# Kernel optimization log

Measured on AMD Instinct MI355X. Metric: run time of the kernel, lower is better.

## Reference

```python
import jax, jax.numpy as jnp
import numpy as np

DIM = 192
NUM_HEADS = 6
KERNELS = [3, 5, 7]
DILATIONS = [1, 2, 3]
NBRANCH = 3
HEADS_B = NUM_HEADS // NBRANCH      # heads per branch = 2
HEAD_DIM = DIM // NUM_HEADS         # 32


def _axis_idx(L, K, d):
    """NATTEN-style neighborhood indices along one axis with dilation.
    Returns (nbr[L,K] absolute neighbor positions, bias[L,K] rpb indices in [0, 2K-2]).
    """
    i = np.arange(L)
    g = i % d                                 # dilation group
    ii = i // d                               # index within subgrid
    Lg = (L - g + d - 1) // d                 # subgrid length of each group
    start = np.clip(ii - K // 2, 0, Lg - K)   # clamp window inside bounds
    ki = np.arange(K)
    nbr = g[:, None] + (start[:, None] + ki[None, :]) * d        # [L,K]
    bias = start[:, None] + ki[None, :] - ii[:, None] + (K - 1)  # [L,K]
    return nbr, bias


def _branch(xb, K, d, rpb):
    # xb: [B,H,W, 3*heads*head_dim] laid out as (3, heads, head_dim)
    B, H, W, _ = xb.shape
    qkv = xb.reshape(B, H, W, 3, HEADS_B, HEAD_DIM).transpose(3, 0, 4, 1, 2, 5)
    q, k, v = qkv[0], qkv[1], qkv[2]          # [B,h,H,W,hd]
    q = q * (HEAD_DIM ** -0.5)
    nh, bh = _axis_idx(H, K, d)
    nw, bw = _axis_idx(W, K, d)
    # gather K x K neighborhoods: [B,h,H,W,K,K,hd]
    k_nb = k[:, :, nh[:, None, :, None], nw[None, :, None, :]]
    attn = jnp.einsum('bhijd,bhijkld->bhijkl', q, k_nb)
    attn = attn + rpb[:, bh[:, None, :, None], bw[None, :, None, :]][None]
    attn = jax.nn.softmax(attn.reshape(B, HEADS_B, H, W, K * K), axis=-1)
    attn = attn.reshape(B, HEADS_B, H, W, K, K)
    v_nb = v[:, :, nh[:, None, :, None], nw[None, :, None, :]]
    y = jnp.einsum('bhijkl,bhijkld->bhijd', attn, v_nb)
    return y.transpose(0, 2, 3, 1, 4).reshape(B, H, W, HEADS_B * HEAD_DIM)


def setup_inputs() -> dict:
    key = jax.random.key(0)
    ks = jax.random.split(key, 8)
    B, H, W = 8, 64, 64
    return {
        'x': jax.random.normal(ks[0], (B, DIM, H, W), jnp.float32),
        'qkv_w': jax.random.normal(ks[1], (3 * DIM, DIM), jnp.float32) * 0.02,
        'qkv_b': jnp.zeros((3 * DIM,), jnp.float32),
        'proj_w': jax.random.normal(ks[2], (DIM, DIM), jnp.float32) * 0.02,
        'proj_b': jnp.zeros((DIM,), jnp.float32),
        'rpb0': jax.random.normal(ks[3], (HEADS_B, 5, 5), jnp.float32) * 0.02,
        'rpb1': jax.random.normal(ks[4], (HEADS_B, 9, 9), jnp.float32) * 0.02,
        'rpb2': jax.random.normal(ks[5], (HEADS_B, 13, 13), jnp.float32) * 0.02,
    }


def reference(x, qkv_w, qkv_b, proj_w, proj_b, rpb0, rpb1, rpb2):
    # x: [B,C,H,W] -> BHWC
    xp = x.transpose(0, 2, 3, 1)
    qkv = xp @ qkv_w.T + qkv_b                 # [B,H,W,3*dim]
    branches = jnp.split(qkv, NBRANCH, axis=-1)  # equal channels (dim divisible by k)
    rpbs = [rpb0, rpb1, rpb2]
    ys = [_branch(branches[i], KERNELS[i], DILATIONS[i], rpbs[i]) for i in range(NBRANCH)]
    out = jnp.concatenate(ys, axis=-1) @ proj_w.T + proj_b
    return out.transpose(0, 3, 1, 2)
```

## Files before the change

### kernel.cpp

```cpp
#include <hip/hip_runtime.h>
#include <stdint.h>

typedef __attribute__((ext_vector_type(4))) float f32x4;
typedef _Float16 half8 __attribute__((ext_vector_type(8)));
typedef _Float16 half2v __attribute__((ext_vector_type(2)));

#define LDK 200
#define QSCALE 0.17677669529663689f

__device__ __forceinline__ float dot2f(unsigned int k2, unsigned int q2, float c) {
#if __has_builtin(__builtin_amdgcn_fdot2)
  return __builtin_amdgcn_fdot2(__builtin_bit_cast(half2v, k2),
                                __builtin_bit_cast(half2v, q2), c, false);
#else
  half2v a = __builtin_bit_cast(half2v, k2), b = __builtin_bit_cast(half2v, q2);
  return c + (float)a.x * (float)b.x + (float)a.y * (float)b.y;
#endif
}

#define MFMA16(A, B, C) __builtin_amdgcn_mfma_f32_16x16x32_f16(A, B, C, 0, 0, 0)

#define GLDS16(gsrc, ldst)                                                      \
  __builtin_amdgcn_global_load_lds(                                             \
      (const __attribute__((address_space(1))) void*)(gsrc),                    \
      (__attribute__((address_space(3))) void*)(ldst), 16, 0, 0)

__global__ __launch_bounds__(256) void prep(
    const float* __restrict__ qw, const float* __restrict__ qb,
    const float* __restrict__ pw,
    _Float16* __restrict__ qwh, float* __restrict__ qbs, _Float16* __restrict__ pwh) {
  int i = blockIdx.x * 256 + threadIdx.x;
  if (i < 13824) {
    int n = i / 24, c = i % 24;
    const float* s = qw + n * 192 + c * 8;
    float sc = ((n % 192) < 64) ? QSCALE : 1.0f;
    half8 h = {(_Float16)(s[0] * sc), (_Float16)(s[1] * sc),
               (_Float16)(s[2] * sc), (_Float16)(s[3] * sc),
               (_Float16)(s[4] * sc), (_Float16)(s[5] * sc),
               (_Float16)(s[6] * sc), (_Float16)(s[7] * sc)};
    *(half8*)(qwh + n * 192 + ((c ^ (n & 7)) << 3)) = h;
  } else if (i < 18432) {
    int k = i - 13824;
    int n = k / 24, c = k % 24;
    const float* s = pw + n * 192 + c * 8;
    half8 h = {(_Float16)s[0], (_Float16)s[1], (_Float16)s[2], (_Float16)s[3],
               (_Float16)s[4], (_Float16)s[5], (_Float16)s[6], (_Float16)s[7]};
    *(half8*)(pwh + n * 192 + ((c ^ (n & 7)) << 3)) = h;
  } else if (i < 19008) {
    int n = i - 18432;
    qbs[n] = qb[n] * (((n % 192) < 64) ? QSCALE : 1.0f);
  }
}

__global__ __launch_bounds__(256) void qkv_gemm(
    const float* __restrict__ x, const _Float16* __restrict__ wh,
    const float* __restrict__ qbs, _Float16* __restrict__ qkv) {
  __shared__ __align__(16) _Float16 Al[64 * LDK];
  __shared__ __align__(16) _Float16 Bsw[2][64 * 192];
  const int t = threadIdx.x;
  const int tm = blockIdx.x;
  const int lane = t & 63, wid = t >> 6;
  const int wm = (wid >> 1) * 32, wn = (wid & 1) * 32;
  const int lr = lane & 15, hi = lane >> 4;
  const int kb = hi * 8, r0 = hi * 4;
  const int xr = lr & 7;

  #pragma unroll
  for (int i = 0; i < 6; ++i)
    GLDS16(wh + (wid * 6 + i) * 512 + lane * 8, &Bsw[0][(wid * 6 + i) * 512]);

  {
    const int bb = tm >> 6, hw0 = (tm & 63) << 6;
    const float* xb = x + (size_t)bb * 192 * 4096 + hw0;
    #pragma unroll
    for (int j = 0; j < 12; ++j) {
      int idx = j * 256 + t;
      int m4 = (idx & 15) * 4, c = idx >> 4;
      float4 v = *(const float4*)(xb + (size_t)c * 4096 + m4);
      Al[(m4 + 0) * LDK + c] = (_Float16)v.x;
      Al[(m4 + 1) * LDK + c] = (_Float16)v.y;
      Al[(m4 + 2) * LDK + c] = (_Float16)v.z;
      Al[(m4 + 3) * LDK + c] = (_Float16)v.w;
    }
  }
  __syncthreads();

  _Float16* opb = qkv + (size_t)(tm * 64) * 576;
  for (int it = 0; it < 9; ++it) {
    if (it < 8) {
      const _Float16* wsrc = wh + (it + 1) * 12288;
      _Float16* bdst = &Bsw[(it + 1) & 1][0];
      #pragma unroll
      for (int i = 0; i < 6; ++i)
        GLDS16(wsrc + (wid * 6 + i) * 512 + lane * 8, bdst + (wid * 6 + i) * 512);
    }
    const _Float16* bc = &Bsw[it & 1][0];

    f32x4 acc[2][2];
    #pragma unroll
    for (int i2 = 0; i2 < 2; ++i2)
      #pragma unroll
      for (int j = 0; j < 2; ++j)
        #pragma unroll
        for (int r = 0; r < 4; ++r) acc[i2][j][r] = 0.0f;

    #pragma unroll
    for (int k6 = 0; k6 < 6; ++k6) {
      half8 a0 = *(const half8*)&Al[(wm + lr) * LDK + k6 * 32 + kb];
      half8 a1 = *(const half8*)&Al[(wm + 16 + lr) * LDK + k6 * 32 + kb];
      const int cs = ((k6 * 4 + hi) ^ xr) << 3;
      half8 b0 = *(const half8*)&bc[(wn + lr) * 192 + cs];
      half8 b1 = *(const half8*)&bc[(wn + 16 + lr) * 192 + cs];
      acc[0][0] = MFMA16(a0, b0, acc[0][0]);
      acc[0][1] = MFMA16(a0, b1, acc[0][1]);
      acc[1][0] = MFMA16(a1, b0, acc[1][0]);
      acc[1][1] = MFMA16(a1, b1, acc[1][1]);
    }

    const int n0 = it * 64;
    const float bs0 = qbs[n0 + wn + lr], bs1 = qbs[n0 + wn + 16 + lr];
    #pragma unroll
    for (int i2 = 0; i2 < 2; ++i2)
      #pragma unroll
      for (int j = 0; j < 2; ++j) {
        int col = n0 + wn + j * 16 + lr;
        float bs = j ? bs1 : bs0;
        #pragma unroll
        for (int r = 0; r < 4; ++r)
          opb[(wm + i2 * 16 + r0 + r) * 576 + col] = (_Float16)(acc[i2][j][r] + bs);
      }
    __syncthreads();
  }
}

template <int K, int DIL>
__device__ __forceinline__ void natten_branch(
    const _Float16* __restrict__ qkv, const float* __restrict__ rpb,
    _Float16* __restrict__ yo, const int branch, const int r,
    unsigned short* __restrict__ smem) {
  constexpr int RW = 2 * K - 1;
  constexpr int H8 = K + 7;
  constexpr int NH = H8 * H8;
  constexpr int NL = (K * K + 3) / 4;
  constexpr int LSTR = 40;
  constexpr int NITER = (NH * 8 + 255) / 256;
  constexpr int DH = 32 / H8, DC = 32 % H8;

  _Float16* Kl = (_Float16*)smem;
  _Float16* Vl = Kl + NH * LSTR;
  _Float16* Ql = Vl + NH * LSTR;
  float* rs = (float*)(Ql + 64 * LSTR);

  const int t = threadIdx.x;
  const int bh = r & 15;
  const int head = bh & 1, bb = bh >> 1;
  const int rr = r >> 4;
  int gh, gw, ti, tj, Lgh, Lgw;
  if (DIL == 1) {
    gh = 0; gw = 0; ti = (rr >> 3) * 8; tj = (rr & 7) * 8; Lgh = 64; Lgw = 64;
  } else if (DIL == 2) {
    int cls = rr >> 4, tile = rr & 15;
    gh = cls >> 1; gw = cls & 1; ti = (tile >> 2) * 8; tj = (tile & 3) * 8;
    Lgh = 32; Lgw = 32;
  } else {
    int cls = rr / 9, tile = rr % 9;
    gh = cls / 3; gw = cls % 3; ti = (tile / 3) * 8; tj = (tile % 3) * 8;
    Lgh = (64 - gh + 2) / 3; Lgw = (64 - gw + 2) / 3;
  }
  const int hoh = max(0, min(ti - K / 2, Lgh - K));
  const int how = max(0, min(tj - K / 2, Lgw - K));

  for (int i = t; i < RW * RW; i += 256) rs[i] = rpb[head * RW * RW + i];

  {
    const _Float16* kvb = qkv + (size_t)bb * 4096 * 576 + branch * 192 + 64 + head * 32;
    const int part = t & 7;
    const int coff = (part & 3) * 8;
    const _Float16* gsrc = kvb + coff + ((part & 4) ? 64 : 0);
    _Float16* dbase = ((part & 4) ? Vl : Kl) + coff;
    int px = t >> 3;
    int hr = px / H8, hc = px - hr * H8;
    #pragma unroll
    for (int itn = 0; itn < NITER; ++itn) {
      if (px < NH) {
        int cr = min(hoh + hr, Lgh - 1), cc = min(how + hc, Lgw - 1);
        int ph = gh + cr * DIL, pw2 = gw + cc * DIL;
        *(uint4*)(dbase + px * LSTR) = *(const uint4*)(gsrc + (size_t)(ph * 64 + pw2) * 576);
      }
      px += 32; hr += DH; hc += DC;
      if (hc >= H8) { hc -= H8; ++hr; }
    }
  }
  {
    int qi = t >> 2, part = t & 3;
    int ci0 = min(ti + (qi >> 3), Lgh - 1), cj0 = min(tj + (qi & 7), Lgw - 1);
    int ph = gh + ci0 * DIL, pw2 = gw + cj0 * DIL;
    const _Float16* src = qkv + (size_t)((size_t)bb * 4096 + ph * 64 + pw2) * 576
                          + branch * 192 + head * 32 + part * 8;
    *(uint4*)(Ql + qi * LSTR + part * 8) = *(const uint4*)src;
  }
  __syncthreads();

  const int qi = t >> 2, sl = t & 3;
  const int ci = ti + (qi >> 3), cj = tj + (qi & 7);
  const bool valid = (ci < Lgh) && (cj < Lgw);

  int s0h = ci - K / 2; if (s0h < 0) s0h = 0; if (s0h > Lgh - K) s0h = Lgh - K;
  int s0w = cj - K / 2; if (s0w < 0) s0w = 0; if (s0w > Lgw - K) s0w = Lgw - K;
  const int rbase = s0h - hoh, cbase = s0w - how;
  const int bhb = s0h - ci + K - 1, bwb = s0w - cj + K - 1;

  unsigned int qh[16];
  #pragma unroll
  for (int u = 0; u < 4; ++u) {
    uint4 v = *(const uint4*)(Ql + qi * LSTR + u * 8);
    qh[u * 4 + 0] = v.x; qh[u * 4 + 1] = v.y; qh[u * 4 + 2] = v.z; qh[u * 4 + 3] = v.w;
  }

  float s[NL];
  float mx = -1e30f;
  #pragma unroll
  for (int j = 0; j < NL; ++j) {
    int n = sl + 4 * j;
    if (n < K * K) {
      int kh = n / K, kw = n % K;
      int lidx = (rbase + kh) * H8 + (cbase + kw);
      const _Float16* kp = Kl + lidx * LSTR;
      float sc = rs[(bhb + kh) * RW + (bwb + kw)];
      #pragma unroll
      for (int u = 0; u < 4; ++u) {
        uint4 kv = *(const uint4*)(kp + u * 8);
        sc = dot2f(kv.x, qh[4 * u + 0], sc);
        sc = dot2f(kv.y, qh[4 * u + 1], sc);
        sc = dot2f(kv.z, qh[4 * u + 2], sc);
        sc = dot2f(kv.w, qh[4 * u + 3], sc);
      }
      s[j] = sc;
      mx = fmaxf(mx, sc);
    } else {
      s[j] = -1e30f;
    }
  }
  mx = fmaxf(mx, __shfl_xor(mx, 1, 64));
  mx = fmaxf(mx, __shfl_xor(mx, 2, 64));

  float pw[NL];
  float l = 0.0f;
  #pragma unroll
  for (int j = 0; j < NL; ++j) { pw[j] = __expf(s[j] - mx); l += pw[j]; }
  l += __shfl_xor(l, 1, 64);
  l += __shfl_xor(l, 2, 64);

  half2v acch[16];
  #pragma unroll
  for (int i = 0; i < 16; ++i) acch[i] = (half2v)(_Float16)0.0f;
  #pragma unroll
  for (int j = 0; j < NL; ++j) {
    int n = sl + 4 * j;
    if (n < K * K) {
      int kh = n / K, kw = n % K;
      int lidx = (rbase + kh) * H8 + (cbase + kw);
      const _Float16* vp = Vl + lidx * LSTR;
      _Float16 ph = (_Float16)pw[j];
      half2v pp = {ph, ph};
      #pragma unroll
      for (int u = 0; u < 4; ++u) {
        uint4 vv = *(const uint4*)(vp + u * 8);
        acch[4 * u + 0] += pp * __builtin_bit_cast(half2v, vv.x);
        acch[4 * u + 1] += pp * __builtin_bit_cast(half2v, vv.y);
        acch[4 * u + 2] += pp * __builtin_bit_cast(half2v, vv.z);
        acch[4 * u + 3] += pp * __builtin_bit_cast(half2v, vv.w);
      }
    }
  }
  #pragma unroll
  for (int st = 1; st <= 2; st <<= 1) {
    #pragma unroll
    for (int i = 0; i < 16; ++i) {
      unsigned int o = __shfl_xor(__builtin_bit_cast(unsigned int, acch[i]), st, 64);
      acch[i] += __builtin_bit_cast(half2v, o);
    }
  }

  if (valid) {
    float inv = 1.0f / l;
    _Float16 ih = (_Float16)inv;
    half2v iv = {ih, ih};
    unsigned int a[16];
    #pragma unroll
    for (int i = 0; i < 16; ++i) a[i] = __builtin_bit_cast(unsigned int, acch[i]);
    uint4 pk;
    unsigned int r0, r1, r2, r3;
    r0 = (sl < 2) ? ((sl == 0) ? a[0] : a[4]) : ((sl == 2) ? a[8] : a[12]);
    r1 = (sl < 2) ? ((sl == 0) ? a[1] : a[5]) : ((sl == 2) ? a[9] : a[13]);
    r2 = (sl < 2) ? ((sl == 0) ? a[2] : a[6]) : ((sl == 2) ? a[10] : a[14]);
    r3 = (sl < 2) ? ((sl == 0) ? a[3] : a[7]) : ((sl == 2) ? a[11] : a[15]);
    pk.x = __builtin_bit_cast(unsigned int, __builtin_bit_cast(half2v, r0) * iv);
    pk.y = __builtin_bit_cast(unsigned int, __builtin_bit_cast(half2v, r1) * iv);
    pk.z = __builtin_bit_cast(unsigned int, __builtin_bit_cast(half2v, r2) * iv);
    pk.w = __builtin_bit_cast(unsigned int, __builtin_bit_cast(half2v, r3) * iv);
    const int p = bb * 4096 + (gh + ci * DIL) * 64 + (gw + cj * DIL);
    *(uint4*)(yo + (size_t)p * 192 + branch * 64 + head * 32 + sl * 8) = pk;
  }
}

__global__ __launch_bounds__(256) void natten_all(
    const _Float16* __restrict__ qkv,
    const float* __restrict__ rpb0, const float* __restrict__ rpb1,
    const float* __restrict__ rpb2, _Float16* __restrict__ yo) {
  __shared__ __align__(16) unsigned short smem[18624];
  const int gid = blockIdx.x;
  if (gid < 1296)       natten_branch<7, 3>(qkv, rpb2, yo, 2, gid, smem);
  else if (gid < 2320)  natten_branch<5, 2>(qkv, rpb1, yo, 1, gid - 1296, smem);
  else                  natten_branch<3, 1>(qkv, rpb0, yo, 0, gid - 2320, smem);
}

__global__ __launch_bounds__(256) void proj_gemm(
    const _Float16* __restrict__ y, const _Float16* __restrict__ wh,
    const float* __restrict__ bias, float* __restrict__ out) {
  __shared__ __align__(16) _Float16 Bl[64 * LDK];
  __shared__ __align__(16) _Float16 Wsw[2][64 * 192];
  const int t = threadIdx.x;
  const int tp = blockIdx.x;
  const int lane = t & 63, wid = t >> 6;
  const int wm = (wid >> 1) * 32, wn = (wid & 1) * 32;
  const int lr = lane & 15, hi = lane >> 4;
  const int kb = hi * 8, r0 = hi * 4;
  const int xr = lr & 7;

  #pragma unroll
  for (int i = 0; i < 6; ++i)
    GLDS16(wh + (wid * 6 + i) * 512 + lane * 8, &Wsw[0][(wid * 6 + i) * 512]);

  {
    const _Float16* ysrc = y + (size_t)(tp * 64) * 192;
    uint4 yv[6];
    #pragma unroll
    for (int q = 0; q < 6; ++q) yv[q] = *(const uint4*)(ysrc + (q * 256 + t) * 8);
    #pragma unroll
    for (int q = 0; q < 6; ++q) {
      int id = q * 256 + t;
      *(uint4*)&Bl[(id / 24) * LDK + (id % 24) * 8] = yv[q];
    }
  }
  __syncthreads();

  const int gp = tp * 64;
  const int bb = gp >> 12, hw0 = gp & 4095;
  float* op = out + (size_t)bb * 192 * 4096 + hw0;

  for (int ci = 0; ci < 3; ++ci) {
    if (ci < 2) {
      const _Float16* wsrc = wh + (ci + 1) * 12288;
      _Float16* wdst = &Wsw[(ci + 1) & 1][0];
      #pragma unroll
      for (int i = 0; i < 6; ++i)
        GLDS16(wsrc + (wid * 6 + i) * 512 + lane * 8, wdst + (wid * 6 + i) * 512);
    }
    const _Float16* wc = &Wsw[ci & 1][0];

    f32x4 acc[2][2];
    #pragma unroll
    for (int i2 = 0; i2 < 2; ++i2)
      #pragma unroll
      for (int j = 0; j < 2; ++j)
        #pragma unroll
        for (int r = 0; r < 4; ++r) acc[i2][j][r] = 0.0f;

    #pragma unroll
    for (int k6 = 0; k6 < 6; ++k6) {
      const int cs = ((k6 * 4 + hi) ^ xr) << 3;
      half8 a0 = *(const half8*)&wc[(wm + lr) * 192 + cs];
      half8 a1 = *(const half8*)&wc[(wm + 16 + lr) * 192 + cs];
      half8 b0 = *(const half8*)&Bl[(wn + lr) * LDK + k6 * 32 + kb];
      half8 b1 = *(const half8*)&Bl[(wn + 16 + lr) * LDK + k6 * 32 + kb];
      acc[0][0] = MFMA16(a0, b0, acc[0][0]);
      acc[0][1] = MFMA16(a0, b1, acc[0][1]);
      acc[1][0] = MFMA16(a1, b0, acc[1][0]);
      acc[1][1] = MFMA16(a1, b1, acc[1][1]);
    }

    const int c0 = ci << 6;
    #pragma unroll
    for (int i2 = 0; i2 < 2; ++i2)
      #pragma unroll
      for (int j = 0; j < 2; ++j) {
        int m = wn + j * 16 + lr;
        #pragma unroll
        for (int r = 0; r < 4; ++r) {
          int c = c0 + wm + i2 * 16 + r0 + r;
          op[(size_t)c * 4096 + m] = acc[i2][j][r] + bias[c];
        }
      }
    __syncthreads();
  }
}

extern "C" void kernel_launch(void* const* d_in, const int* in_sizes, int n_in,
                              void* d_out, int out_size, void* d_ws, size_t ws_size,
                              hipStream_t stream) {
  const float* x      = (const float*)d_in[0];
  const float* qkv_w  = (const float*)d_in[1];
  const float* qkv_b  = (const float*)d_in[2];
  const float* proj_w = (const float*)d_in[3];
  const float* proj_b = (const float*)d_in[4];
  const float* rpb0   = (const float*)d_in[5];
  const float* rpb1   = (const float*)d_in[6];
  const float* rpb2   = (const float*)d_in[7];

  _Float16* qkv = (_Float16*)d_ws;
  _Float16* yb  = qkv + (size_t)32768 * 576;
  _Float16* qwh = yb + (size_t)32768 * 192;
  _Float16* pwh = qwh + 110592;
  float*    qbs = (float*)(pwh + 36864);
  float* out = (float*)d_out;

  prep<<<dim3(75), 256, 0, stream>>>(qkv_w, qkv_b, proj_w, qwh, qbs, pwh);
  qkv_gemm<<<dim3(512), 256, 0, stream>>>(x, qwh, qbs, qkv);
  natten_all<<<dim3(3344), 256, 0, stream>>>(qkv, rpb0, rpb1, rpb2, yb);
  proj_gemm<<<dim3(512), 256, 0, stream>>>(yb, pwh, proj_b, out);
}
```

Baseline: 135.6 us.

## Interleave K/V in shared memory, load Q directly to registers, use exp2 softmax

The NATTEN kernel now stores K and V interleaved per neighbor pixel in a single LDS array with a 72-half stride, replacing separate K/V arrays. Q is loaded straight from global memory into registers instead of being staged through LDS, which drops one LDS buffer and shrinks shared memory per block, possibly raising occupancy. The log2(e) factor is folded into the Q scale and the relative position bias so softmax can use exp2f. Risks are LDS bank conflicts with the new stride and uncoalesced per-thread global Q reads.

```diff
diff --git a/kernel.cpp b/kernel.cpp
--- a/kernel.cpp
+++ b/kernel.cpp
@@ -6,7 +6,8 @@
 typedef _Float16 half2v __attribute__((ext_vector_type(2)));
 
 #define LDK 200
-#define QSCALE 0.17677669529663689f
+#define LOG2E 1.4426950408889634f
+#define QSCALE2 (0.17677669529663689f * 1.4426950408889634f)
 
 __device__ __forceinline__ float dot2f(unsigned int k2, unsigned int q2, float c) {
 #if __has_builtin(__builtin_amdgcn_fdot2)
@@ -33,7 +34,7 @@
   if (i < 13824) {
     int n = i / 24, c = i % 24;
     const float* s = qw + n * 192 + c * 8;
-    float sc = ((n % 192) < 64) ? QSCALE : 1.0f;
+    float sc = ((n % 192) < 64) ? QSCALE2 : 1.0f;
     half8 h = {(_Float16)(s[0] * sc), (_Float16)(s[1] * sc),
                (_Float16)(s[2] * sc), (_Float16)(s[3] * sc),
                (_Float16)(s[4] * sc), (_Float16)(s[5] * sc),
@@ -48,7 +49,7 @@
     *(half8*)(pwh + n * 192 + ((c ^ (n & 7)) << 3)) = h;
   } else if (i < 19008) {
     int n = i - 18432;
-    qbs[n] = qb[n] * (((n % 192) < 64) ? QSCALE : 1.0f);
+    qbs[n] = qb[n] * (((n % 192) < 64) ? QSCALE2 : 1.0f);
   }
 }
 
@@ -142,14 +143,12 @@
   constexpr int H8 = K + 7;
   constexpr int NH = H8 * H8;
   constexpr int NL = (K * K + 3) / 4;
-  constexpr int LSTR = 40;
+  constexpr int LSTR = 72;
   constexpr int NITER = (NH * 8 + 255) / 256;
   constexpr int DH = 32 / H8, DC = 32 % H8;
 
-  _Float16* Kl = (_Float16*)smem;
-  _Float16* Vl = Kl + NH * LSTR;
-  _Float16* Ql = Vl + NH * LSTR;
-  float* rs = (float*)(Ql + 64 * LSTR);
+  _Float16* KV = (_Float16*)smem;
+  float* rs = (float*)(KV + NH * LSTR);
 
   const int t = threadIdx.x;
   const int bh = r & 15;
@@ -170,14 +169,13 @@
   const int hoh = max(0, min(ti - K / 2, Lgh - K));
   const int how = max(0, min(tj - K / 2, Lgw - K));
 
-  for (int i = t; i < RW * RW; i += 256) rs[i] = rpb[head * RW * RW + i];
+  for (int i = t; i < RW * RW; i += 256) rs[i] = rpb[head * RW * RW + i] * LOG2E;
 
   {
     const _Float16* kvb = qkv + (size_t)bb * 4096 * 576 + branch * 192 + 64 + head * 32;
     const int part = t & 7;
-    const int coff = (part & 3) * 8;
-    const _Float16* gsrc = kvb + coff + ((part & 4) ? 64 : 0);
-    _Float16* dbase = ((part & 4) ? Vl : Kl) + coff;
+    const _Float16* gsrc = kvb + (part & 3) * 8 + ((part & 4) ? 64 : 0);
+    _Float16* dbase = KV + part * 8;
     int px = t >> 3;
     int hr = px / H8, hc = px - hr * H8;
     #pragma unroll
@@ -191,31 +189,29 @@
       if (hc >= H8) { hc -= H8; ++hr; }
     }
   }
-  {
-    int qi = t >> 2, part = t & 3;
-    int ci0 = min(ti + (qi >> 3), Lgh - 1), cj0 = min(tj + (qi & 7), Lgw - 1);
-    int ph = gh + ci0 * DIL, pw2 = gw + cj0 * DIL;
-    const _Float16* src = qkv + (size_t)((size_t)bb * 4096 + ph * 64 + pw2) * 576
-                          + branch * 192 + head * 32 + part * 8;
-    *(uint4*)(Ql + qi * LSTR + part * 8) = *(const uint4*)src;
-  }
-  __syncthreads();
 
   const int qi = t >> 2, sl = t & 3;
   const int ci = ti + (qi >> 3), cj = tj + (qi & 7);
   const bool valid = (ci < Lgh) && (cj < Lgw);
+  const int cic = min(ci, Lgh - 1), cjc = min(cj, Lgw - 1);
+  const int p = bb * 4096 + (gh + cic * DIL) * 64 + (gw + cjc * DIL);
+
+  unsigned int qh[16];
+  {
+    const _Float16* qp = qkv + (size_t)p * 576 + branch * 192 + head * 32;
+    #pragma unroll
+    for (int u = 0; u < 4; ++u) {
+      uint4 v = *(const uint4*)(qp + u * 8);
+      qh[u * 4 + 0] = v.x; qh[u * 4 + 1] = v.y; qh[u * 4 + 2] = v.z; qh[u * 4 + 3] = v.w;
+    }
+  }
 
   int s0h = ci - K / 2; if (s0h < 0) s0h = 0; if (s0h > Lgh - K) s0h = Lgh - K;
   int s0w = cj - K / 2; if (s0w < 0) s0w = 0; if (s0w > Lgw - K) s0w = Lgw - K;
   const int rbase = s0h - hoh, cbase = s0w - how;
   const int bhb = s0h - ci + K - 1, bwb = s0w - cj + K - 1;
 
-  unsigned int qh[16];
-  #pragma unroll
-  for (int u = 0; u < 4; ++u) {
-    uint4 v = *(const uint4*)(Ql + qi * LSTR + u * 8);
-    qh[u * 4 + 0] = v.x; qh[u * 4 + 1] = v.y; qh[u * 4 + 2] = v.z; qh[u * 4 + 3] = v.w;
-  }
+  __syncthreads();
 
   float s[NL];
   float mx = -1e30f;
@@ -225,7 +221,7 @@
     if (n < K * K) {
       int kh = n / K, kw = n % K;
       int lidx = (rbase + kh) * H8 + (cbase + kw);
-      const _Float16* kp = Kl + lidx * LSTR;
+      const _Float16* kp = KV + lidx * LSTR;
       float sc = rs[(bhb + kh) * RW + (bwb + kw)];
       #pragma unroll
       for (int u = 0; u < 4; ++u) {
@@ -244,10 +240,9 @@
   mx = fmaxf(mx, __shfl_xor(mx, 1, 64));
   mx = fmaxf(mx, __shfl_xor(mx, 2, 64));
 
-  float pw[NL];
   float l = 0.0f;
   #pragma unroll
-  for (int j = 0; j < NL; ++j) { pw[j] = __expf(s[j] - mx); l += pw[j]; }
+  for (int j = 0; j < NL; ++j) { float pv = exp2f(s[j] - mx); s[j] = pv; l += pv; }
   l += __shfl_xor(l, 1, 64);
   l += __shfl_xor(l, 2, 64);
 
@@ -260,8 +255,8 @@
     if (n < K * K) {
       int kh = n / K, kw = n % K;
       int lidx = (rbase + kh) * H8 + (cbase + kw);
-      const _Float16* vp = Vl + lidx * LSTR;
-      _Float16 ph = (_Float16)pw[j];
+      const _Float16* vp = KV + lidx * LSTR + 32;
+      _Float16 ph = (_Float16)s[j];
       half2v pp = {ph, ph};
       #pragma unroll
       for (int u = 0; u < 4; ++u) {
@@ -299,7 +294,6 @@
     pk.y = __builtin_bit_cast(unsigned int, __builtin_bit_cast(half2v, r1) * iv);
     pk.z = __builtin_bit_cast(unsigned int, __builtin_bit_cast(half2v, r2) * iv);
     pk.w = __builtin_bit_cast(unsigned int, __builtin_bit_cast(half2v, r3) * iv);
-    const int p = bb * 4096 + (gh + ci * DIL) * 64 + (gw + cj * DIL);
     *(uint4*)(yo + (size_t)p * 192 + branch * 64 + head * 32 + sl * 8) = pk;
   }
 }
@@ -308,7 +302,7 @@
     const _Float16* __restrict__ qkv,
     const float* __restrict__ rpb0, const float* __restrict__ rpb1,
     const float* __restrict__ rpb2, _Float16* __restrict__ yo) {
-  __shared__ __align__(16) unsigned short smem[18624];
+  __shared__ __align__(16) unsigned short smem[14464];
   const int gid = blockIdx.x;
   if (gid < 1296)       natten_branch<7, 3>(qkv, rpb2, yo, 2, gid, smem);
   else if (gid < 2320)  natten_branch<5, 2>(qkv, rpb1, yo, 1, gid - 1296, smem);
```

Measured after the change: 135.3 us. About the same (-0.2%).
